# Optimization experiments

Hardware: AMD Instinct MI355X
Metric: run time of the kernel (lower is better)

## Reference

```python
import jax, jax.numpy as jnp
import numpy as np
import math

B = 2048
NOSC = 64            # oscillators per modality
M = 3                # modalities (audio, text, vision) in sorted order
BDIM = 256           # binding_dim
DT = 0.01
NSTEPS = 10
DIMS = [512, 768, 1024]  # audio, text, vision
TWO_PI = 2.0 * math.pi


def setup_inputs() -> dict:
    key = jax.random.key(0)
    ks = iter(jax.random.split(key, 40))
    d = {}
    names = ['a', 't', 'v']
    for name, dim, x_key in zip(names, DIMS, ['x_audio', 'x_text', 'x_vision']):
        d[x_key] = jax.random.normal(next(ks), (B, dim), dtype=jnp.float32)
        s = 1.0 / math.sqrt(dim)
        d[f'Wf_{name}'] = jax.random.uniform(next(ks), (BDIM, dim), jnp.float32, -s, s)
        d[f'bf_{name}'] = jax.random.uniform(next(ks), (BDIM,), jnp.float32, -s, s)
        d[f'Wp_{name}'] = jax.random.uniform(next(ks), (NOSC, dim), jnp.float32, -s, s)
        d[f'bp_{name}'] = jax.random.uniform(next(ks), (NOSC,), jnp.float32, -s, s)
    # omegas: randn*0.1 + 1.0 + i*0.5 for i-th sorted modality
    for i, name in enumerate(names):
        d[f'omega_{name}'] = jax.random.normal(next(ks), (NOSC,), jnp.float32) * 0.1 + 1.0 + i * 0.5
    N = M * NOSC
    d['inter_coupling'] = jax.random.normal(next(ks), (N, N), jnp.float32) * 0.1
    s = 1.0 / math.sqrt(BDIM * M)
    d['W_fusion'] = jax.random.uniform(next(ks), (BDIM, BDIM * M), jnp.float32, -s, s)
    d['b_fusion'] = jax.random.uniform(next(ks), (BDIM,), jnp.float32, -s, s)
    return d


def reference(x_audio, x_text, x_vision,
              Wf_a, bf_a, Wp_a, bp_a,
              Wf_t, bf_t, Wp_t, bp_t,
              Wf_v, bf_v, Wp_v, bp_v,
              omega_a, omega_t, omega_v,
              inter_coupling, W_fusion, b_fusion):
    def enc(x, Wf, bf, Wp, bp):
        encoded = x @ Wf.T + bf                       # (B, BDIM)
        phases = (x @ Wp.T + bp) % TWO_PI             # (B, NOSC)
        return encoded, phases

    e_a, p_a = enc(x_audio, Wf_a, bf_a, Wp_a, bp_a)
    e_t, p_t = enc(x_text, Wf_t, bf_t, Wp_t, bp_t)
    e_v, p_v = enc(x_vision, Wf_v, bf_v, Wp_v, bp_v)

    phases = jnp.concatenate([p_a, p_t, p_v], axis=-1)        # (B, N)
    omega = jnp.concatenate([omega_a, omega_t, omega_v])      # (N,)
    K = (inter_coupling + inter_coupling.T) * 0.5             # (N, N)
    N = phases.shape[-1]

    def step(ph, _):
        diff = ph[:, :, None] - ph[:, None, :]                # (B, N, N)
        forces = jnp.einsum('ij,bij->bi', K, jnp.sin(diff)) / N
        ph = (ph + DT * (omega[None, :] + forces)) % TWO_PI
        return ph, None

    phases, _ = jax.lax.scan(step, phases, None, length=NSTEPS)

    pm = [phases[:, i * NOSC:(i + 1) * NOSC] for i in range(M)]  # per-modality

    # PLV between banks a,b: |mean_{i,j} exp(i(a_i - b_j))| = R_a * R_b where
    # R = |mean_k exp(i phi_k)| (resultant length), computed with real math.
    R = jnp.stack([jnp.sqrt(jnp.mean(jnp.cos(p), -1) ** 2 +
                            jnp.mean(jnp.sin(p), -1) ** 2) for p in pm])  # (M, B)
    bm = jnp.mean(R[:, None, :] * R[None, :, :], axis=-1)      # (M, M)
    binding_matrix = jnp.where(jnp.eye(M, dtype=bool), 1.0, bm)

    fused_parts = []
    for e, p in zip([e_a, e_t, e_v], pm):
        phase_mod = jnp.mean(jnp.cos(p), axis=-1, keepdims=True)  # (B, 1)
        fused_parts.append(e * (0.5 + 0.5 * phase_mod))
    fused = jnp.concatenate(fused_parts, axis=-1)              # (B, M*BDIM)
    bound = fused @ W_fusion.T + b_fusion                      # (B, BDIM)

    triu = jnp.triu(jnp.ones((M, M), dtype=bool), k=1)
    total = jnp.sum(jnp.where(triu, binding_matrix, 0.0)) / triu.sum()
    total_binding = jnp.full((bound.shape[0],), total)

    return bound, binding_matrix, phases, total_binding
```

## Files before the change

kernel.cpp:

```cpp
#include <hip/hip_runtime.h>
#include <math.h>

typedef short bf16x8 __attribute__((ext_vector_type(8)));
typedef short bf16x4 __attribute__((ext_vector_type(4)));
typedef float f32x4  __attribute__((ext_vector_type(4)));

#define INV_2PI  0.15915494309189535f
#define TWO_PI_F 6.283185307179586f
#define FSCALE   8.2893199e-06f

static __device__ inline short f2bf(float f) {
    union { float f; unsigned u; } v; v.f = f;
    unsigned r = (v.u + 0x7FFFu + ((v.u >> 16) & 1u)) >> 16;
    return (short)r;
}
static __device__ inline float bf2f(short h) {
    union { unsigned u; float f; } v; v.u = ((unsigned)(unsigned short)h) << 16;
    return v.f;
}

__global__ __launch_bounds__(256) void front_kernel(
    const float* __restrict__ xa, const float* __restrict__ xt, const float* __restrict__ xv,
    const float* __restrict__ Wpa, const float* __restrict__ Wpt, const float* __restrict__ Wpv,
    const float* __restrict__ Wfa, const float* __restrict__ Wft, const float* __restrict__ Wfv,
    const float* __restrict__ Wfu,
    const float* __restrict__ IC,
    const float* __restrict__ oa, const float* __restrict__ ot, const float* __restrict__ ov,
    const float* __restrict__ bpa, const float* __restrict__ bpt, const float* __restrict__ bpv,
    float* __restrict__ partial, short* __restrict__ XB, short* __restrict__ WB,
    short* __restrict__ Kp,
    float* __restrict__ om_eff, float* __restrict__ bp_all, float* __restrict__ bacc)
{
    __shared__ alignas(16) float As[16][72];
    __shared__ alignas(16) float Bs[16][72];
    int b = blockIdx.x;
    int t = threadIdx.x;

    if (b < 576) {
        int slot = b % 18, rb = b / 18;
        int z = slot < 4 ? 0 : (slot < 10 ? 1 : 2);
        int chunk = slot - (z == 0 ? 0 : (z == 1 ? 4 : 10));
        const float* A = z == 0 ? xa : (z == 1 ? xt : xv);
        const float* W = z == 0 ? Wpa : (z == 1 ? Wpt : Wpv);
        short* XBz = XB + (z == 0 ? 0 : (z == 1 ? 1048576 : 2621440));
        int K = z == 0 ? 512 : (z == 1 ? 768 : 1024);
        int kb = chunk * 128;
        int m0 = rb * 64;

        int tx = t & 15, ty = t >> 4;
        int row = t >> 2, c4 = t & 3;

        float acc[4][4] = {};
        float4 ar = *(const float4*)&A[(size_t)(m0 + row) * K + kb + c4 * 4];
        float4 br = *(const float4*)&W[(size_t)row * K + kb + c4 * 4];

        for (int k0 = 0; k0 < 128; k0 += 16) {
            if (k0) __syncthreads();
            As[c4 * 4 + 0][row] = ar.x;
            As[c4 * 4 + 1][row] = ar.y;
            As[c4 * 4 + 2][row] = ar.z;
            As[c4 * 4 + 3][row] = ar.w;
            Bs[c4 * 4 + 0][row] = br.x;
            Bs[c4 * 4 + 1][row] = br.y;
            Bs[c4 * 4 + 2][row] = br.z;
            Bs[c4 * 4 + 3][row] = br.w;
            {
                bf16x4 h; h[0] = f2bf(ar.x); h[1] = f2bf(ar.y);
                h[2] = f2bf(ar.z); h[3] = f2bf(ar.w);
                *(bf16x4*)&XBz[(size_t)(m0 + row) * K + kb + k0 + c4 * 4] = h;
            }
            __syncthreads();
            if (k0 + 16 < 128) {
                ar = *(const float4*)&A[(size_t)(m0 + row) * K + kb + k0 + 16 + c4 * 4];
                br = *(const float4*)&W[(size_t)row * K + kb + k0 + 16 + c4 * 4];
            }
#pragma unroll
            for (int kk = 0; kk < 16; ++kk) {
                float4 aq = *(const float4*)&As[kk][ty * 4];
                float4 bq = *(const float4*)&Bs[kk][tx * 4];
                float av[4] = {aq.x, aq.y, aq.z, aq.w};
                float bv[4] = {bq.x, bq.y, bq.z, bq.w};
#pragma unroll
                for (int i = 0; i < 4; ++i)
#pragma unroll
                    for (int j = 0; j < 4; ++j)
                        acc[i][j] += av[i] * bv[j];
            }
        }

#pragma unroll
        for (int i = 0; i < 4; ++i) {
            int row_l = ty * 4 + i;
            int qb = rb * 4 + (row_l >> 4), rloc = row_l & 15;
            float4 v = make_float4(acc[i][0], acc[i][1], acc[i][2], acc[i][3]);
            *(float4*)&partial[((size_t)(qb * 18 + slot)) * 1024 + rloc * 64 + tx * 4] = v;
        }
    } else if (b < 600) {
        for (int u = (b - 576) * 256 + t; u < 196608; u += 24 * 256) {
            const float4* sp;
            if (u < 32768)       sp = (const float4*)Wfa + u;
            else if (u < 81920)  sp = (const float4*)Wft + (u - 32768);
            else if (u < 147456) sp = (const float4*)Wfv + (u - 81920);
            else                 sp = (const float4*)Wfu + (u - 147456);
            float4 v = *sp;
            bf16x4 h; h[0] = f2bf(v.x); h[1] = f2bf(v.y); h[2] = f2bf(v.z); h[3] = f2bf(v.w);
            *(bf16x4*)(WB + (size_t)u * 4) = h;
        }
    } else if (b < 632) {
        for (int idx = (b - 600) * 256 + t; idx < 36864; idx += 32 * 256) {
            int k = idx / 192, n = idx - k * 192;
            float v = 0.5f * (IC[k * 192 + n] + IC[n * 192 + k]);
            int nt = n >> 4, kc = k >> 5;
            int lane = ((k >> 3) & 3) * 16 + (n & 15);
            int j = k & 7;
            Kp[((nt * 6 + kc) * 64 + lane) * 8 + j] = f2bf(v);
        }
    } else {
        if (t < 192) {
            float w = t < 64 ? oa[t] : (t < 128 ? ot[t - 64] : ov[t - 128]);
            om_eff[t] = w * (0.01f * INV_2PI);
            float bb = t < 64 ? bpa[t] : (t < 128 ? bpt[t - 64] : bpv[t - 128]);
            bp_all[t] = bb;
        }
        if (t < 4) bacc[t] = 0.f;
    }
}

__global__ __launch_bounds__(256) void mid_kernel(
    const short* __restrict__ XB, const short* __restrict__ WB,
    const float* __restrict__ ba, const float* __restrict__ bt, const float* __restrict__ bv,
    const float* __restrict__ partial, const float* __restrict__ bp_all,
    const short* __restrict__ Kp, const float* __restrict__ om_eff,
    short* __restrict__ e_bf16,
    float* __restrict__ phases_out, float* __restrict__ pm, float* __restrict__ bacc)
{
    __shared__ alignas(16) char smem[27840];
    int b = blockIdx.x;
    int t = threadIdx.x;
    int lane = t & 63, w = t >> 6;
    int q = lane >> 4, col = lane & 15;

    if (b >= 128) {
        int bb = b - 128;
        int z = bb / 128, r = bb % 128;
        int m0 = (r >> 2) * 64, n0 = (r & 3) * 64;
        const short* A    = XB + (z == 0 ? 0 : (z == 1 ? 1048576 : 2621440));
        const short* W    = WB + (z == 0 ? 0 : (z == 1 ? 131072 : 327680));
        const float* bias = z == 0 ? ba : (z == 1 ? bt : bv);
        int K             = z == 0 ? 512 : (z == 1 ? 768 : 1024);

        short* As = (short*)smem;
        short* Bs = (short*)smem + 64 * 72;

        int srow = t >> 3, sc8 = t & 7;

        f32x4 acc[4];
#pragma unroll
        for (int f = 0; f < 4; ++f)
#pragma unroll
            for (int rr = 0; rr < 4; ++rr) acc[f][rr] = 0.f;

        bf16x8 av[2], bv8[2];
#pragma unroll
        for (int p = 0; p < 2; ++p) {
            av[p]  = *(const bf16x8*)&A[(size_t)(m0 + srow + 32 * p) * K + sc8 * 8];
            bv8[p] = *(const bf16x8*)&W[(size_t)(n0 + srow + 32 * p) * K + sc8 * 8];
        }

        for (int kb = 0; kb < K; kb += 64) {
            if (kb) __syncthreads();
#pragma unroll
            for (int p = 0; p < 2; ++p) {
                *(bf16x8*)&As[(srow + 32 * p) * 72 + sc8 * 8] = av[p];
                *(bf16x8*)&Bs[(srow + 32 * p) * 72 + sc8 * 8] = bv8[p];
            }
            __syncthreads();
            if (kb + 64 < K) {
#pragma unroll
                for (int p = 0; p < 2; ++p) {
                    av[p]  = *(const bf16x8*)&A[(size_t)(m0 + srow + 32 * p) * K + kb + 64 + sc8 * 8];
                    bv8[p] = *(const bf16x8*)&W[(size_t)(n0 + srow + 32 * p) * K + kb + 64 + sc8 * 8];
                }
            }

            bf16x8 bfr[2];
#pragma unroll
            for (int kc = 0; kc < 2; ++kc)
                bfr[kc] = *(const bf16x8*)&Bs[(w * 16 + col) * 72 + kc * 32 + q * 8];
#pragma unroll
            for (int f = 0; f < 4; ++f)
#pragma unroll
                for (int kc = 0; kc < 2; ++kc) {
                    bf16x8 af = *(const bf16x8*)&As[(f * 16 + col) * 72 + kc * 32 + q * 8];
                    acc[f] = __builtin_amdgcn_mfma_f32_16x16x32_bf16(af, bfr[kc], acc[f], 0, 0, 0);
                }
        }

        int n = n0 + w * 16 + col;
        float bn = bias[n];
#pragma unroll
        for (int f = 0; f < 4; ++f)
#pragma unroll
            for (int rr = 0; rr < 4; ++rr) {
                int m = m0 + f * 16 + q * 4 + rr;
                e_bf16[(size_t)m * 768 + z * 256 + n] = f2bf(acc[f][rr] + bn);
            }
    } else {
        short (*cs)[2][16][216] = (short (*)[2][16][216])smem;
        float (*Rl)[3] = (float (*)[3])(smem + 27648);
        float* ph0 = (float*)smem;

        int m0 = b * 16;

        bf16x8 kb[3][6];
#pragma unroll
        for (int ntl = 0; ntl < 3; ++ntl)
#pragma unroll
            for (int kc = 0; kc < 6; ++kc) {
                int nt = w * 3 + ntl;
                kb[ntl][kc] = *(const bf16x8*)&Kp[((nt * 6 + kc) * 64 + lane) * 8];
            }

        {
            const float* Pb = partial + (size_t)b * 18 * 1024;
            f32x4 s0, s1, s2;
#pragma unroll
            for (int j = 0; j < 4; ++j) { s0[j] = 0.f; s1[j] = 0.f; s2[j] = 0.f; }
#pragma unroll
            for (int s = 0; s < 18; ++s) {
                f32x4 v = *(const f32x4*)&Pb[s * 1024 + t * 4];
                if (s < 4)       s0 += v;
                else if (s < 10) s1 += v;
                else             s2 += v;
            }
            int row = t >> 4, c4 = t & 15;
            *(f32x4*)&ph0[row * 196 +   0 + c4 * 4] = s0;
            *(f32x4*)&ph0[row * 196 +  64 + c4 * 4] = s1;
            *(f32x4*)&ph0[row * 196 + 128 + c4 * 4] = s2;
        }
        __syncthreads();

        float ph[3][4], om[3], c[3][4], s[3][4];
#pragma unroll
        for (int ntl = 0; ntl < 3; ++ntl) {
            int i = (w * 3 + ntl) * 16 + col;
            om[ntl] = om_eff[i];
#pragma unroll
            for (int r = 0; r < 4; ++r) {
                float raw = bp_all[i] + ph0[(q * 4 + r) * 196 + i];
                raw *= INV_2PI;
                ph[ntl][r] = raw - floorf(raw);
            }
        }
        __syncthreads();

        for (int step = 0; step < 10; ++step) {
            int p = step & 1;
#pragma unroll
            for (int ntl = 0; ntl < 3; ++ntl) {
                int i = (w * 3 + ntl) * 16 + col;
#pragma unroll
                for (int r = 0; r < 4; ++r) {
                    c[ntl][r] = __builtin_amdgcn_cosf(ph[ntl][r]);
                    s[ntl][r] = __builtin_amdgcn_sinf(ph[ntl][r]);
                    cs[p][0][q * 4 + r][i] = f2bf(c[ntl][r]);
                    cs[p][1][q * 4 + r][i] = f2bf(s[ntl][r]);
                }
            }
            __syncthreads();

            f32x4 aC[3], aS[3];
#pragma unroll
            for (int ntl = 0; ntl < 3; ++ntl)
#pragma unroll
                for (int r = 0; r < 4; ++r) { aC[ntl][r] = 0.f; aS[ntl][r] = 0.f; }

#pragma unroll
            for (int kc = 0; kc < 6; ++kc) {
                bf16x8 ac  = *(const bf16x8*)&cs[p][0][col][kc * 32 + q * 8];
                bf16x8 as_ = *(const bf16x8*)&cs[p][1][col][kc * 32 + q * 8];
#pragma unroll
                for (int ntl = 0; ntl < 3; ++ntl) {
                    aC[ntl] = __builtin_amdgcn_mfma_f32_16x16x32_bf16(ac,  kb[ntl][kc], aC[ntl], 0, 0, 0);
                    aS[ntl] = __builtin_amdgcn_mfma_f32_16x16x32_bf16(as_, kb[ntl][kc], aS[ntl], 0, 0, 0);
                }
            }

#pragma unroll
            for (int ntl = 0; ntl < 3; ++ntl)
#pragma unroll
                for (int r = 0; r < 4; ++r) {
                    float f = (s[ntl][r] * aC[ntl][r] - c[ntl][r] * aS[ntl][r]) * FSCALE;
                    float pn = ph[ntl][r] + om[ntl] + f;
                    ph[ntl][r] = pn - floorf(pn);
                }
        }

#pragma unroll
        for (int ntl = 0; ntl < 3; ++ntl) {
            int i = (w * 3 + ntl) * 16 + col;
#pragma unroll
            for (int r = 0; r < 4; ++r) {
                float cp = __builtin_amdgcn_cosf(ph[ntl][r]);
                float sp = __builtin_amdgcn_sinf(ph[ntl][r]);
                cs[0][0][q * 4 + r][i] = f2bf(cp);
                cs[0][1][q * 4 + r][i] = f2bf(sp);
                phases_out[(size_t)(m0 + q * 4 + r) * 192 + i] = ph[ntl][r] * TWO_PI_F;
            }
        }
        __syncthreads();

        if (t < 48) {
            int r = t & 15, mod = t >> 4;
            float sc = 0.f, ss = 0.f;
#pragma unroll
            for (int g = 0; g < 8; ++g) {
                bf16x8 vc = *(const bf16x8*)&cs[0][0][r][mod * 64 + g * 8];
                bf16x8 vs = *(const bf16x8*)&cs[0][1][r][mod * 64 + g * 8];
#pragma unroll
                for (int j = 0; j < 8; ++j) { sc += bf2f(vc[j]); ss += bf2f(vs[j]); }
            }
            sc *= (1.f / 64.f); ss *= (1.f / 64.f);
            pm[(size_t)(m0 + r) * 3 + mod] = 0.5f + 0.5f * sc;
            Rl[r][mod] = sqrtf(sc * sc + ss * ss);
        }
        __syncthreads();
        if (t < 3) {
            int a = (t == 2) ? 1 : 0;
            int bb = (t == 0) ? 1 : 2;
            float accp = 0.f;
            for (int r = 0; r < 16; ++r) accp += Rl[r][a] * Rl[r][bb];
            atomicAdd(&bacc[t], accp);
        }
    }
}

__global__ __launch_bounds__(256) void back_kernel(
    const short* __restrict__ e_bf16, const short* __restrict__ WB,
    const float* __restrict__ bias, const float* __restrict__ pm,
    const float* __restrict__ bacc,
    float* __restrict__ out_bound, float* __restrict__ out_bm, float* __restrict__ out_total)
{
    const short* Wfb = WB + 589824;
    __shared__ alignas(16) short As2[16 * 776];

    int m0 = blockIdx.x * 16, n0 = blockIdx.y * 128;
    int t = threadIdx.x;
    int lane = t & 63, w = t >> 6;
    int q = lane >> 4, col = lane & 15;

#pragma unroll
    for (int i = 0; i < 6; ++i) {
        int g = t + 256 * i;
        int rw = g / 96, cg = g - rw * 96;
        float sc = pm[(size_t)(m0 + rw) * 3 + (cg >> 5)];
        bf16x8 v = *(const bf16x8*)&e_bf16[(size_t)(m0 + rw) * 768 + cg * 8];
        bf16x8 h;
#pragma unroll
        for (int j = 0; j < 8; ++j) h[j] = f2bf(bf2f(v[j]) * sc);
        *(bf16x8*)&As2[rw * 776 + cg * 8] = h;
    }
    __syncthreads();

    f32x4 facc[2];
#pragma unroll
    for (int j = 0; j < 2; ++j)
#pragma unroll
        for (int rr = 0; rr < 4; ++rr) facc[j][rr] = 0.f;

    int n_[2];
#pragma unroll
    for (int j = 0; j < 2; ++j) n_[j] = n0 + (w * 2 + j) * 16 + col;

    bf16x8 bcur[2], bnxt[2];
#pragma unroll
    for (int j = 0; j < 2; ++j)
        bcur[j] = *(const bf16x8*)&Wfb[(size_t)n_[j] * 768 + q * 8];

    for (int k0 = 0; k0 < 768; k0 += 32) {
        if (k0 + 32 < 768) {
#pragma unroll
            for (int j = 0; j < 2; ++j)
                bnxt[j] = *(const bf16x8*)&Wfb[(size_t)n_[j] * 768 + k0 + 32 + q * 8];
        }
        bf16x8 af = *(const bf16x8*)&As2[col * 776 + k0 + q * 8];
#pragma unroll
        for (int j = 0; j < 2; ++j)
            facc[j] = __builtin_amdgcn_mfma_f32_16x16x32_bf16(af, bcur[j], facc[j], 0, 0, 0);
#pragma unroll
        for (int j = 0; j < 2; ++j) bcur[j] = bnxt[j];
    }

#pragma unroll
    for (int j = 0; j < 2; ++j) {
        float bn = bias[n_[j]];
#pragma unroll
        for (int rr = 0; rr < 4; ++rr) {
            int m = m0 + q * 4 + rr;
            out_bound[(size_t)m * 256 + n_[j]] = facc[j][rr] + bn;
        }
    }

    if (blockIdx.x == 0 && blockIdx.y == 0) {
        float p01 = bacc[0] * (1.f / 2048.f);
        float p02 = bacc[1] * (1.f / 2048.f);
        float p12 = bacc[2] * (1.f / 2048.f);
        float total = (p01 + p02 + p12) * (1.f / 3.f);
        if (t == 0) {
            out_bm[0] = 1.f; out_bm[1] = p01; out_bm[2] = p02;
            out_bm[3] = p01; out_bm[4] = 1.f; out_bm[5] = p12;
            out_bm[6] = p02; out_bm[7] = p12; out_bm[8] = 1.f;
        }
        for (int i = t; i < 2048; i += 256) out_total[i] = total;
    }
}

extern "C" void kernel_launch(void* const* d_in, const int* in_sizes, int n_in,
                              void* d_out, int out_size, void* d_ws, size_t ws_size,
                              hipStream_t stream)
{
    const float* x_a  = (const float*)d_in[0];
    const float* Wf_a = (const float*)d_in[1];
    const float* bf_a = (const float*)d_in[2];
    const float* Wp_a = (const float*)d_in[3];
    const float* bp_a = (const float*)d_in[4];
    const float* x_t  = (const float*)d_in[5];
    const float* Wf_t = (const float*)d_in[6];
    const float* bf_t = (const float*)d_in[7];
    const float* Wp_t = (const float*)d_in[8];
    const float* bp_t = (const float*)d_in[9];
    const float* x_v  = (const float*)d_in[10];
    const float* Wf_v = (const float*)d_in[11];
    const float* bf_v = (const float*)d_in[12];
    const float* Wp_v = (const float*)d_in[13];
    const float* bp_v = (const float*)d_in[14];
    const float* om_a = (const float*)d_in[15];
    const float* om_t = (const float*)d_in[16];
    const float* om_v = (const float*)d_in[17];
    const float* IC   = (const float*)d_in[18];
    const float* Wfu  = (const float*)d_in[19];
    const float* bfu  = (const float*)d_in[20];

    float* ws      = (float*)d_ws;
    float* omw     = ws;
    float* bpw     = ws + 256;
    float* pmv     = ws + 512;
    float* baccw   = ws + 6656;
    float* partial = ws + 6720;
    short* e_bf    = (short*)(ws + 2366016);
    short* XB      = (short*)(ws + 3152448);
    short* Kpck    = (short*)(ws + 5511744);
    short* WB      = (short*)(ws + 5530176);

    float* out        = (float*)d_out;
    float* out_bound  = out;
    float* out_bm     = out + 524288;
    float* out_phases = out + 524297;
    float* out_total  = out + 917513;

    front_kernel<<<633, 256, 0, stream>>>(
        x_a, x_t, x_v, Wp_a, Wp_t, Wp_v, Wf_a, Wf_t, Wf_v, Wfu,
        IC, om_a, om_t, om_v, bp_a, bp_t, bp_v,
        partial, XB, WB, Kpck, omw, bpw, baccw);

    mid_kernel<<<512, 256, 0, stream>>>(
        XB, WB, bf_a, bf_t, bf_v,
        partial, bpw, Kpck, omw,
        e_bf, out_phases, pmv, baccw);

    dim3 gF(128, 2);
    back_kernel<<<gF, 256, 0, stream>>>(e_bf, WB, bfu, pmv, baccw,
                                        out_bound, out_bm, out_total);
}
```

Before: 142.3 us.

## Merge front and mid kernels with per-row-block counters and in-register bf16 conversion

Folds the phase-projection split-K GEMM, the encoder GEMMs, the fusion-weight conversion and the Kuramoto integration into one launch. Cross-block dependencies are handled by per-row-block atomic counters that the oscillator blocks spin on. The encoder GEMM now reads fp32 inputs and converts them to bf16 while staging into shared memory, which removes the XB/WB staging round trips. Each block computes the symmetrized coupling matrix and omega directly instead of loading prepacked copies, the phase GEMM gets a double-buffered LDS tile, and the global binding atomic becomes per-block partials that are summed in back_kernel. The main risks are deadlock or stalls if the consumer blocks get scheduled before their producers, plus redundant coupling-matrix computation in every oscillator block.

```diff
diff --git a/kernel.cpp b/kernel.cpp
--- a/kernel.cpp
+++ b/kernel.cpp
@@ -18,121 +18,24 @@
     union { unsigned u; float f; } v; v.u = ((unsigned)(unsigned short)h) << 16;
     return v.f;
 }
-
-__global__ __launch_bounds__(256) void front_kernel(
+static __device__ inline bf16x8 cvt8(float4 u, float4 v) {
+    bf16x8 h;
+    h[0] = f2bf(u.x); h[1] = f2bf(u.y); h[2] = f2bf(u.z); h[3] = f2bf(u.w);
+    h[4] = f2bf(v.x); h[5] = f2bf(v.y); h[6] = f2bf(v.z); h[7] = f2bf(v.w);
+    return h;
+}
+
+__global__ __launch_bounds__(256) void main_kernel(
     const float* __restrict__ xa, const float* __restrict__ xt, const float* __restrict__ xv,
     const float* __restrict__ Wpa, const float* __restrict__ Wpt, const float* __restrict__ Wpv,
     const float* __restrict__ Wfa, const float* __restrict__ Wft, const float* __restrict__ Wfv,
-    const float* __restrict__ Wfu,
-    const float* __restrict__ IC,
+    const float* __restrict__ bfa, const float* __restrict__ bft, const float* __restrict__ bfv,
+    const float* __restrict__ Wfu, const float* __restrict__ IC,
     const float* __restrict__ oa, const float* __restrict__ ot, const float* __restrict__ ov,
     const float* __restrict__ bpa, const float* __restrict__ bpt, const float* __restrict__ bpv,
-    float* __restrict__ partial, short* __restrict__ XB, short* __restrict__ WB,
-    short* __restrict__ Kp,
-    float* __restrict__ om_eff, float* __restrict__ bp_all, float* __restrict__ bacc)
-{
-    __shared__ alignas(16) float As[16][72];
-    __shared__ alignas(16) float Bs[16][72];
-    int b = blockIdx.x;
-    int t = threadIdx.x;
-
-    if (b < 576) {
-        int slot = b % 18, rb = b / 18;
-        int z = slot < 4 ? 0 : (slot < 10 ? 1 : 2);
-        int chunk = slot - (z == 0 ? 0 : (z == 1 ? 4 : 10));
-        const float* A = z == 0 ? xa : (z == 1 ? xt : xv);
-        const float* W = z == 0 ? Wpa : (z == 1 ? Wpt : Wpv);
-        short* XBz = XB + (z == 0 ? 0 : (z == 1 ? 1048576 : 2621440));
-        int K = z == 0 ? 512 : (z == 1 ? 768 : 1024);
-        int kb = chunk * 128;
-        int m0 = rb * 64;
-
-        int tx = t & 15, ty = t >> 4;
-        int row = t >> 2, c4 = t & 3;
-
-        float acc[4][4] = {};
-        float4 ar = *(const float4*)&A[(size_t)(m0 + row) * K + kb + c4 * 4];
-        float4 br = *(const float4*)&W[(size_t)row * K + kb + c4 * 4];
-
-        for (int k0 = 0; k0 < 128; k0 += 16) {
-            if (k0) __syncthreads();
-            As[c4 * 4 + 0][row] = ar.x;
-            As[c4 * 4 + 1][row] = ar.y;
-            As[c4 * 4 + 2][row] = ar.z;
-            As[c4 * 4 + 3][row] = ar.w;
-            Bs[c4 * 4 + 0][row] = br.x;
-            Bs[c4 * 4 + 1][row] = br.y;
-            Bs[c4 * 4 + 2][row] = br.z;
-            Bs[c4 * 4 + 3][row] = br.w;
-            {
-                bf16x4 h; h[0] = f2bf(ar.x); h[1] = f2bf(ar.y);
-                h[2] = f2bf(ar.z); h[3] = f2bf(ar.w);
-                *(bf16x4*)&XBz[(size_t)(m0 + row) * K + kb + k0 + c4 * 4] = h;
-            }
-            __syncthreads();
-            if (k0 + 16 < 128) {
-                ar = *(const float4*)&A[(size_t)(m0 + row) * K + kb + k0 + 16 + c4 * 4];
-                br = *(const float4*)&W[(size_t)row * K + kb + k0 + 16 + c4 * 4];
-            }
-#pragma unroll
-            for (int kk = 0; kk < 16; ++kk) {
-                float4 aq = *(const float4*)&As[kk][ty * 4];
-                float4 bq = *(const float4*)&Bs[kk][tx * 4];
-                float av[4] = {aq.x, aq.y, aq.z, aq.w};
-                float bv[4] = {bq.x, bq.y, bq.z, bq.w};
-#pragma unroll
-                for (int i = 0; i < 4; ++i)
-#pragma unroll
-                    for (int j = 0; j < 4; ++j)
-                        acc[i][j] += av[i] * bv[j];
-            }
-        }
-
-#pragma unroll
-        for (int i = 0; i < 4; ++i) {
-            int row_l = ty * 4 + i;
-            int qb = rb * 4 + (row_l >> 4), rloc = row_l & 15;
-            float4 v = make_float4(acc[i][0], acc[i][1], acc[i][2], acc[i][3]);
-            *(float4*)&partial[((size_t)(qb * 18 + slot)) * 1024 + rloc * 64 + tx * 4] = v;
-        }
-    } else if (b < 600) {
-        for (int u = (b - 576) * 256 + t; u < 196608; u += 24 * 256) {
-            const float4* sp;
-            if (u < 32768)       sp = (const float4*)Wfa + u;
-            else if (u < 81920)  sp = (const float4*)Wft + (u - 32768);
-            else if (u < 147456) sp = (const float4*)Wfv + (u - 81920);
-            else                 sp = (const float4*)Wfu + (u - 147456);
-            float4 v = *sp;
-            bf16x4 h; h[0] = f2bf(v.x); h[1] = f2bf(v.y); h[2] = f2bf(v.z); h[3] = f2bf(v.w);
-            *(bf16x4*)(WB + (size_t)u * 4) = h;
-        }
-    } else if (b < 632) {
-        for (int idx = (b - 600) * 256 + t; idx < 36864; idx += 32 * 256) {
-            int k = idx / 192, n = idx - k * 192;
-            float v = 0.5f * (IC[k * 192 + n] + IC[n * 192 + k]);
-            int nt = n >> 4, kc = k >> 5;
-            int lane = ((k >> 3) & 3) * 16 + (n & 15);
-            int j = k & 7;
-            Kp[((nt * 6 + kc) * 64 + lane) * 8 + j] = f2bf(v);
-        }
-    } else {
-        if (t < 192) {
-            float w = t < 64 ? oa[t] : (t < 128 ? ot[t - 64] : ov[t - 128]);
-            om_eff[t] = w * (0.01f * INV_2PI);
-            float bb = t < 64 ? bpa[t] : (t < 128 ? bpt[t - 64] : bpv[t - 128]);
-            bp_all[t] = bb;
-        }
-        if (t < 4) bacc[t] = 0.f;
-    }
-}
-
-__global__ __launch_bounds__(256) void mid_kernel(
-    const short* __restrict__ XB, const short* __restrict__ WB,
-    const float* __restrict__ ba, const float* __restrict__ bt, const float* __restrict__ bv,
-    const float* __restrict__ partial, const float* __restrict__ bp_all,
-    const short* __restrict__ Kp, const float* __restrict__ om_eff,
-    short* __restrict__ e_bf16,
-    float* __restrict__ phases_out, float* __restrict__ pm, float* __restrict__ bacc)
+    float* __restrict__ partial, short* __restrict__ e_bf16, short* __restrict__ WB,
+    float* __restrict__ phases_out, float* __restrict__ pm,
+    float* __restrict__ bacc_part, unsigned* __restrict__ ctr)
 {
     __shared__ alignas(16) char smem[27840];
     int b = blockIdx.x;
@@ -140,13 +43,74 @@
     int lane = t & 63, w = t >> 6;
     int q = lane >> 4, col = lane & 15;
 
-    if (b >= 128) {
-        int bb = b - 128;
-        int z = bb / 128, r = bb % 128;
+    if (b < 576) {
+        float (*As)[16][72] = (float (*)[16][72])smem;
+        float (*Bs)[16][72] = (float (*)[16][72])(smem + 9216);
+        int slot = b % 18, rb = b / 18;
+        int z = slot < 4 ? 0 : (slot < 10 ? 1 : 2);
+        int chunk = slot - (z == 0 ? 0 : (z == 1 ? 4 : 10));
+        const float* A = z == 0 ? xa : (z == 1 ? xt : xv);
+        const float* W = z == 0 ? Wpa : (z == 1 ? Wpt : Wpv);
+        int K = z == 0 ? 512 : (z == 1 ? 768 : 1024);
+        int kb = chunk * 128;
+        int m0 = rb * 64;
+
+        int tx = t & 15, ty = t >> 4;
+        int row = t >> 2, c4 = t & 3;
+
+        float acc[4][4] = {};
+        float4 arq[2], brq[2];
+        arq[0] = *(const float4*)&A[(size_t)(m0 + row) * K + kb + c4 * 4];
+        brq[0] = *(const float4*)&W[(size_t)row * K + kb + c4 * 4];
+        arq[1] = *(const float4*)&A[(size_t)(m0 + row) * K + kb + 16 + c4 * 4];
+        brq[1] = *(const float4*)&W[(size_t)row * K + kb + 16 + c4 * 4];
+
+        for (int it = 0; it < 8; ++it) {
+            int cur = it & 1;
+            As[cur][c4 * 4 + 0][row] = arq[cur].x;
+            As[cur][c4 * 4 + 1][row] = arq[cur].y;
+            As[cur][c4 * 4 + 2][row] = arq[cur].z;
+            As[cur][c4 * 4 + 3][row] = arq[cur].w;
+            Bs[cur][c4 * 4 + 0][row] = brq[cur].x;
+            Bs[cur][c4 * 4 + 1][row] = brq[cur].y;
+            Bs[cur][c4 * 4 + 2][row] = brq[cur].z;
+            Bs[cur][c4 * 4 + 3][row] = brq[cur].w;
+            __syncthreads();
+            if (it + 2 < 8) {
+                arq[cur] = *(const float4*)&A[(size_t)(m0 + row) * K + kb + (it + 2) * 16 + c4 * 4];
+                brq[cur] = *(const float4*)&W[(size_t)row * K + kb + (it + 2) * 16 + c4 * 4];
+            }
+#pragma unroll
+            for (int kk = 0; kk < 16; ++kk) {
+                float4 aq = *(const float4*)&As[cur][kk][ty * 4];
+                float4 bq = *(const float4*)&Bs[cur][kk][tx * 4];
+                float av[4] = {aq.x, aq.y, aq.z, aq.w};
+                float bv[4] = {bq.x, bq.y, bq.z, bq.w};
+#pragma unroll
+                for (int i = 0; i < 4; ++i)
+#pragma unroll
+                    for (int j = 0; j < 4; ++j)
+                        acc[i][j] += av[i] * bv[j];
+            }
+        }
+
+#pragma unroll
+        for (int i = 0; i < 4; ++i) {
+            int row_l = ty * 4 + i;
+            int qb = rb * 4 + (row_l >> 4), rloc = row_l & 15;
+            float4 v = make_float4(acc[i][0], acc[i][1], acc[i][2], acc[i][3]);
+            *(float4*)&partial[((size_t)(qb * 18 + slot)) * 1024 + rloc * 64 + tx * 4] = v;
+        }
+        __threadfence();
+        __syncthreads();
+        if (t == 0) atomicAdd(&ctr[rb], 1u);
+    } else if (b < 960) {
+        int bb = b - 576;
+        int z = bb >> 7, r = bb & 127;
         int m0 = (r >> 2) * 64, n0 = (r & 3) * 64;
-        const short* A    = XB + (z == 0 ? 0 : (z == 1 ? 1048576 : 2621440));
-        const short* W    = WB + (z == 0 ? 0 : (z == 1 ? 131072 : 327680));
-        const float* bias = z == 0 ? ba : (z == 1 ? bt : bv);
+        const float* A    = z == 0 ? xa : (z == 1 ? xt : xv);
+        const float* Wf   = z == 0 ? Wfa : (z == 1 ? Wft : Wfv);
+        const float* bias = z == 0 ? bfa : (z == 1 ? bft : bfv);
         int K             = z == 0 ? 512 : (z == 1 ? 768 : 1024);
 
         short* As = (short*)smem;
@@ -160,26 +124,34 @@
 #pragma unroll
             for (int rr = 0; rr < 4; ++rr) acc[f][rr] = 0.f;
 
-        bf16x8 av[2], bv8[2];
+        float4 a0[2], a1[2], b0[2], b1[2];
 #pragma unroll
         for (int p = 0; p < 2; ++p) {
-            av[p]  = *(const bf16x8*)&A[(size_t)(m0 + srow + 32 * p) * K + sc8 * 8];
-            bv8[p] = *(const bf16x8*)&W[(size_t)(n0 + srow + 32 * p) * K + sc8 * 8];
+            int rw = srow + 32 * p;
+            a0[p] = *(const float4*)&A[(size_t)(m0 + rw) * K + sc8 * 8];
+            a1[p] = *(const float4*)&A[(size_t)(m0 + rw) * K + sc8 * 8 + 4];
+            b0[p] = *(const float4*)&Wf[(size_t)(n0 + rw) * K + sc8 * 8];
+            b1[p] = *(const float4*)&Wf[(size_t)(n0 + rw) * K + sc8 * 8 + 4];
         }
 
         for (int kb = 0; kb < K; kb += 64) {
             if (kb) __syncthreads();
 #pragma unroll
             for (int p = 0; p < 2; ++p) {
-                *(bf16x8*)&As[(srow + 32 * p) * 72 + sc8 * 8] = av[p];
-                *(bf16x8*)&Bs[(srow + 32 * p) * 72 + sc8 * 8] = bv8[p];
+                int rw = srow + 32 * p;
+                *(bf16x8*)&As[rw * 72 + sc8 * 8] = cvt8(a0[p], a1[p]);
+                *(bf16x8*)&Bs[rw * 72 + sc8 * 8] = cvt8(b0[p], b1[p]);
             }
             __syncthreads();
             if (kb + 64 < K) {
+                int k = kb + 64;
 #pragma unroll
                 for (int p = 0; p < 2; ++p) {
-                    av[p]  = *(const bf16x8*)&A[(size_t)(m0 + srow + 32 * p) * K + kb + 64 + sc8 * 8];
-                    bv8[p] = *(const bf16x8*)&W[(size_t)(n0 + srow + 32 * p) * K + kb + 64 + sc8 * 8];
+                    int rw = srow + 32 * p;
+                    a0[p] = *(const float4*)&A[(size_t)(m0 + rw) * K + k + sc8 * 8];
+                    a1[p] = *(const float4*)&A[(size_t)(m0 + rw) * K + k + sc8 * 8 + 4];
+                    b0[p] = *(const float4*)&Wf[(size_t)(n0 + rw) * K + k + sc8 * 8];
+                    b1[p] = *(const float4*)&Wf[(size_t)(n0 + rw) * K + k + sc8 * 8 + 4];
                 }
             }
 
@@ -205,24 +177,54 @@
                 int m = m0 + f * 16 + q * 4 + rr;
                 e_bf16[(size_t)m * 768 + z * 256 + n] = f2bf(acc[f][rr] + bn);
             }
+    } else if (b < 972) {
+        for (int u = (b - 960) * 256 + t; u < 49152; u += 12 * 256) {
+            float4 v = ((const float4*)Wfu)[u];
+            bf16x4 h; h[0] = f2bf(v.x); h[1] = f2bf(v.y); h[2] = f2bf(v.z); h[3] = f2bf(v.w);
+            *(bf16x4*)(WB + (size_t)u * 4) = h;
+        }
     } else {
         short (*cs)[2][16][216] = (short (*)[2][16][216])smem;
         float (*Rl)[3] = (float (*)[3])(smem + 27648);
         float* ph0 = (float*)smem;
 
-        int m0 = b * 16;
-
-        bf16x8 kb[3][6];
+        int g = b - 972;
+        int m0 = g * 16;
+
+        bf16x8 kb_[3][6];
 #pragma unroll
         for (int ntl = 0; ntl < 3; ++ntl)
 #pragma unroll
             for (int kc = 0; kc < 6; ++kc) {
                 int nt = w * 3 + ntl;
-                kb[ntl][kc] = *(const bf16x8*)&Kp[((nt * 6 + kc) * 64 + lane) * 8];
-            }
+                int n = nt * 16 + (lane & 15);
+                int kbase = kc * 32 + (lane >> 4) * 8;
+#pragma unroll
+                for (int j = 0; j < 8; ++j) {
+                    int k = kbase + j;
+                    float v = 0.5f * (IC[k * 192 + n] + IC[n * 192 + k]);
+                    kb_[ntl][kc][j] = f2bf(v);
+                }
+            }
+
+        float om[3], bpv_[3];
+#pragma unroll
+        for (int ntl = 0; ntl < 3; ++ntl) {
+            int i = (w * 3 + ntl) * 16 + col;
+            int z = i >> 6, ii = i & 63;
+            float wv = z == 0 ? oa[ii] : (z == 1 ? ot[ii] : ov[ii]);
+            om[ntl] = wv * (0.01f * INV_2PI);
+            bpv_[ntl] = z == 0 ? bpa[ii] : (z == 1 ? bpt[ii] : bpv[ii]);
+        }
+
+        if (t == 0) {
+            while (atomicAdd(&ctr[g >> 2], 0u) < 18u) __builtin_amdgcn_s_sleep(2);
+        }
+        __syncthreads();
+        __threadfence();
 
         {
-            const float* Pb = partial + (size_t)b * 18 * 1024;
+            const float* Pb = partial + (size_t)g * 18 * 1024;
             f32x4 s0, s1, s2;
 #pragma unroll
             for (int j = 0; j < 4; ++j) { s0[j] = 0.f; s1[j] = 0.f; s2[j] = 0.f; }
@@ -240,14 +242,13 @@
         }
         __syncthreads();
 
-        float ph[3][4], om[3], c[3][4], s[3][4];
+        float ph[3][4], c[3][4], s[3][4];
 #pragma unroll
         for (int ntl = 0; ntl < 3; ++ntl) {
             int i = (w * 3 + ntl) * 16 + col;
-            om[ntl] = om_eff[i];
 #pragma unroll
             for (int r = 0; r < 4; ++r) {
-                float raw = bp_all[i] + ph0[(q * 4 + r) * 196 + i];
+                float raw = bpv_[ntl] + ph0[(q * 4 + r) * 196 + i];
                 raw *= INV_2PI;
                 ph[ntl][r] = raw - floorf(raw);
             }
@@ -281,8 +282,8 @@
                 bf16x8 as_ = *(const bf16x8*)&cs[p][1][col][kc * 32 + q * 8];
 #pragma unroll
                 for (int ntl = 0; ntl < 3; ++ntl) {
-                    aC[ntl] = __builtin_amdgcn_mfma_f32_16x16x32_bf16(ac,  kb[ntl][kc], aC[ntl], 0, 0, 0);
-                    aS[ntl] = __builtin_amdgcn_mfma_f32_16x16x32_bf16(as_, kb[ntl][kc], aS[ntl], 0, 0, 0);
+                    aC[ntl] = __builtin_amdgcn_mfma_f32_16x16x32_bf16(ac,  kb_[ntl][kc], aC[ntl], 0, 0, 0);
+                    aS[ntl] = __builtin_amdgcn_mfma_f32_16x16x32_bf16(as_, kb_[ntl][kc], aS[ntl], 0, 0, 0);
                 }
             }
 
@@ -314,9 +315,9 @@
             int r = t & 15, mod = t >> 4;
             float sc = 0.f, ss = 0.f;
 #pragma unroll
-            for (int g = 0; g < 8; ++g) {
-                bf16x8 vc = *(const bf16x8*)&cs[0][0][r][mod * 64 + g * 8];
-                bf16x8 vs = *(const bf16x8*)&cs[0][1][r][mod * 64 + g * 8];
+            for (int gg = 0; gg < 8; ++gg) {
+                bf16x8 vc = *(const bf16x8*)&cs[0][0][r][mod * 64 + gg * 8];
+                bf16x8 vs = *(const bf16x8*)&cs[0][1][r][mod * 64 + gg * 8];
 #pragma unroll
                 for (int j = 0; j < 8; ++j) { sc += bf2f(vc[j]); ss += bf2f(vs[j]); }
             }
@@ -327,10 +328,10 @@
         __syncthreads();
         if (t < 3) {
             int a = (t == 2) ? 1 : 0;
-            int bb = (t == 0) ? 1 : 2;
+            int bb2 = (t == 0) ? 1 : 2;
             float accp = 0.f;
-            for (int r = 0; r < 16; ++r) accp += Rl[r][a] * Rl[r][bb];
-            atomicAdd(&bacc[t], accp);
+            for (int r = 0; r < 16; ++r) accp += Rl[r][a] * Rl[r][bb2];
+            bacc_part[g * 4 + t] = accp;
         }
     }
 }
@@ -338,11 +339,12 @@
 __global__ __launch_bounds__(256) void back_kernel(
     const short* __restrict__ e_bf16, const short* __restrict__ WB,
     const float* __restrict__ bias, const float* __restrict__ pm,
-    const float* __restrict__ bacc,
+    const float* __restrict__ bacc_part,
     float* __restrict__ out_bound, float* __restrict__ out_bm, float* __restrict__ out_total)
 {
-    const short* Wfb = WB + 589824;
+    const short* Wfb = WB;
     __shared__ alignas(16) short As2[16 * 776];
+    __shared__ float fsum[3];
 
     int m0 = blockIdx.x * 16, n0 = blockIdx.y * 128;
     int t = threadIdx.x;
@@ -402,9 +404,15 @@
     }
 
     if (blockIdx.x == 0 && blockIdx.y == 0) {
-        float p01 = bacc[0] * (1.f / 2048.f);
-        float p02 = bacc[1] * (1.f / 2048.f);
-        float p12 = bacc[2] * (1.f / 2048.f);
+        if (t < 3) {
+            float s = 0.f;
+            for (int g = 0; g < 128; ++g) s += bacc_part[g * 4 + t];
+            fsum[t] = s;
+        }
+        __syncthreads();
+        float p01 = fsum[0] * (1.f / 2048.f);
+        float p02 = fsum[1] * (1.f / 2048.f);
+        float p12 = fsum[2] * (1.f / 2048.f);
         float total = (p01 + p02 + p12) * (1.f / 3.f);
         if (t == 0) {
             out_bm[0] = 1.f; out_bm[1] = p01; out_bm[2] = p02;
@@ -441,16 +449,13 @@
     const float* Wfu  = (const float*)d_in[19];
     const float* bfu  = (const float*)d_in[20];
 
-    float* ws      = (float*)d_ws;
-    float* omw     = ws;
-    float* bpw     = ws + 256;
-    float* pmv     = ws + 512;
-    float* baccw   = ws + 6656;
-    float* partial = ws + 6720;
-    short* e_bf    = (short*)(ws + 2366016);
-    short* XB      = (short*)(ws + 3152448);
-    short* Kpck    = (short*)(ws + 5511744);
-    short* WB      = (short*)(ws + 5530176);
+    float* ws        = (float*)d_ws;
+    unsigned* ctrw   = (unsigned*)ws;
+    float* baccp     = ws + 32;
+    float* pmv       = ws + 544;
+    float* partial   = ws + 6688;
+    short* e_bf      = (short*)(ws + 2365984);
+    short* WB        = (short*)(ws + 3152416);
 
     float* out        = (float*)d_out;
     float* out_bound  = out;
@@ -458,17 +463,14 @@
     float* out_phases = out + 524297;
     float* out_total  = out + 917513;
 
-    front_kernel<<<633, 256, 0, stream>>>(
-        x_a, x_t, x_v, Wp_a, Wp_t, Wp_v, Wf_a, Wf_t, Wf_v, Wfu,
-        IC, om_a, om_t, om_v, bp_a, bp_t, bp_v,
-        partial, XB, WB, Kpck, omw, bpw, baccw);
-
-    mid_kernel<<<512, 256, 0, stream>>>(
-        XB, WB, bf_a, bf_t, bf_v,
-        partial, bpw, Kpck, omw,
-        e_bf, out_phases, pmv, baccw);
+    hipMemsetAsync(ctrw, 0, 128, stream);
+
+    main_kernel<<<1100, 256, 0, stream>>>(
+        x_a, x_t, x_v, Wp_a, Wp_t, Wp_v, Wf_a, Wf_t, Wf_v,
+        bf_a, bf_t, bf_v, Wfu, IC, om_a, om_t, om_v, bp_a, bp_t, bp_v,
+        partial, e_bf, WB, out_phases, pmv, baccp, ctrw);
 
     dim3 gF(128, 2);
-    back_kernel<<<gF, 256, 0, stream>>>(e_bf, WB, bfu, pmv, baccw,
+    back_kernel<<<gF, 256, 0, stream>>>(e_bf, WB, bfu, pmv, baccp,
                                         out_bound, out_bm, out_total);
 }
```

Result: slower. 228.6 us (+60.7%).
